# Kernel tuning notes

Measured on AMD Instinct MI355X. Metric: run time of the kernel, lower is better.

Reference implementation:

```python
import jax, jax.numpy as jnp
import numpy as np


def setup_inputs() -> dict:
    key = jax.random.key(0)
    k1, k2, k3, k4 = jax.random.split(key, 4)
    B, S, K, N = 2, 1024, 4096, 4096
    x = jax.random.normal(k1, (B, S, K), dtype=jnp.float32)
    # int8 weights in [-128, 127]
    weight = jax.random.randint(k2, (N, K), -128, 128, dtype=jnp.int8)
    # per-output-channel dequant scales (small positive values)
    scales = jax.random.uniform(k3, (N,), dtype=jnp.float32, minval=0.005, maxval=0.02)
    bias = jax.random.normal(k4, (N,), dtype=jnp.float32) * 0.1
    return {"x": x, "weight": weight, "scales": scales, "bias": bias}


def reference(x, weight, scales, bias):
    # F.linear(x, weight.to(x.dtype)): [B,S,K] @ [N,K]^T -> [B,S,N]
    w = weight.astype(x.dtype)
    y = jnp.einsum('bsk,nk->bsn', x, w)
    # per-output-channel scale + bias epilogue
    return y * scales + bias
```

## Files before the change

kernel.cpp:

```cpp
#include <hip/hip_runtime.h>
#include <hip/hip_bf16.h>
#include <stdint.h>

#define M_DIM 2048
#define N_DIM 4096
#define K_DIM 4096

#define BM 128
#define BN 128
#define BK 128

#define ATILE (BM * BK)
#define BTILE (BN * BK)

typedef __attribute__((ext_vector_type(4))) int   int4v;
typedef __attribute__((ext_vector_type(4))) float f32x4;

__device__ __forceinline__ void load_lds16(const void* g, void* l) {
    __builtin_amdgcn_global_load_lds(
        (const __attribute__((address_space(1))) void*)g,
        (__attribute__((address_space(3))) void*)l,
        16, 0, 0);
}

__global__ __launch_bounds__(256) void quant_x(const float* __restrict__ x,
                                               int8_t* __restrict__ Aq,
                                               float* __restrict__ sx) {
    const int row = blockIdx.x;
    const int tid = threadIdx.x;
    const float4* xr = (const float4*)(x + (size_t)row * K_DIM);

    float4 v[4];
    float mx = 0.f;
#pragma unroll
    for (int p = 0; p < 4; p++) {
        v[p] = xr[p * 256 + tid];
        mx = fmaxf(mx, fmaxf(fmaxf(fabsf(v[p].x), fabsf(v[p].y)),
                             fmaxf(fabsf(v[p].z), fabsf(v[p].w))));
    }
#pragma unroll
    for (int off = 32; off >= 1; off >>= 1)
        mx = fmaxf(mx, __shfl_xor(mx, off, 64));

    __shared__ float wmax[4];
    __shared__ float smax;
    if ((tid & 63) == 0) wmax[tid >> 6] = mx;
    __syncthreads();
    if (tid == 0) {
        float m = fmaxf(fmaxf(wmax[0], wmax[1]), fmaxf(wmax[2], wmax[3]));
        m = fmaxf(m, 1e-20f);
        smax = m;
        sx[row] = m * (1.0f / 127.0f);
    }
    __syncthreads();
    const float inv = 127.0f / smax;

    int* out = (int*)Aq + (size_t)row * (K_DIM / 4);
#pragma unroll
    for (int p = 0; p < 4; p++) {
        int q0 = (int)__builtin_rintf(v[p].x * inv);
        int q1 = (int)__builtin_rintf(v[p].y * inv);
        int q2 = (int)__builtin_rintf(v[p].z * inv);
        int q3 = (int)__builtin_rintf(v[p].w * inv);
        q0 = max(-127, min(127, q0)); q1 = max(-127, min(127, q1));
        q2 = max(-127, min(127, q2)); q3 = max(-127, min(127, q3));
        out[p * 256 + tid] = (q0 & 255) | ((q1 & 255) << 8) |
                             ((q2 & 255) << 16) | ((q3 & 255) << 24);
    }
}

__global__ __launch_bounds__(256) void cvt_w8(const int* __restrict__ w,
                                              int8_t* __restrict__ Bq) {
    size_t i = ((size_t)blockIdx.x * 256 + threadIdx.x) * 16;
    int4 a0 = *(const int4*)(w + i);
    int4 a1 = *(const int4*)(w + i + 4);
    int4 a2 = *(const int4*)(w + i + 8);
    int4 a3 = *(const int4*)(w + i + 12);
    uint4 t;
    t.x = (a0.x & 255) | ((a0.y & 255) << 8) | ((a0.z & 255) << 16) | ((a0.w & 255) << 24);
    t.y = (a1.x & 255) | ((a1.y & 255) << 8) | ((a1.z & 255) << 16) | ((a1.w & 255) << 24);
    t.z = (a2.x & 255) | ((a2.y & 255) << 8) | ((a2.z & 255) << 16) | ((a2.w & 255) << 24);
    t.w = (a3.x & 255) | ((a3.y & 255) << 8) | ((a3.z & 255) << 16) | ((a3.w & 255) << 24);
    *(uint4*)(Bq + i) = t;
}


__global__ __launch_bounds__(512, 4) void gemm_bt_i8(
    const int8_t* __restrict__ A,
    const int8_t* __restrict__ B,
    const float*  __restrict__ sx,
    const float*  __restrict__ scales,
    const float*  __restrict__ bias,
    float* __restrict__ C)
{
    __shared__ __align__(16) int8_t As[2 * ATILE];
    __shared__ __align__(16) int8_t Bs[2 * BTILE];

    const int tid  = threadIdx.x;
    const int bm   = blockIdx.y;
    const int bn   = blockIdx.x;
    const int lane = tid & 63;
    const int wave = tid >> 6;
    const int wm   = (wave >> 2) * 64;
    const int wn   = (wave & 3) * 32;
    const int l16  = lane & 15;
    const int quad = lane >> 4;
    const int swz  = l16 & 7;

    const int srow = tid >> 3;
    const int cgp  = tid & 7;
    const int cgl  = cgp ^ (srow & 7);

    const int8_t* ga0 = A + (size_t)(bm * BM + srow)      * K_DIM + cgl * 16;
    const int8_t* ga1 = A + (size_t)(bm * BM + 64 + srow) * K_DIM + cgl * 16;
    const int8_t* gb0 = B + (size_t)(bn * BN + srow)      * K_DIM + cgl * 16;
    const int8_t* gb1 = B + (size_t)(bn * BN + 64 + srow) * K_DIM + cgl * 16;
    const int la0 = srow * BK + cgp * 16;
    const int la1 = (64 + srow) * BK + cgp * 16;

    load_lds16(ga0, As + la0);
    load_lds16(ga1, As + la1);
    load_lds16(gb0, Bs + la0);
    load_lds16(gb1, Bs + la1);

    int4v acc[4][2] = {};

    int cur = 0;
    for (int k0 = 0; k0 < K_DIM; k0 += BK, cur ^= 1) {
        __syncthreads();

        const int kn = k0 + BK;
        if (kn < K_DIM) {
            const int nb = (cur ^ 1);
            load_lds16(ga0 + kn, As + nb * ATILE + la0);
            load_lds16(ga1 + kn, As + nb * ATILE + la1);
            load_lds16(gb0 + kn, Bs + nb * BTILE + la0);
            load_lds16(gb1 + kn, Bs + nb * BTILE + la1);
        }

        const int8_t* Ab = As + cur * ATILE;
        const int8_t* Bb = Bs + cur * BTILE;

#pragma unroll
        for (int h = 0; h < 2; h++) {
            const int cp = (h * 4 + quad) ^ swz;
            int4v af[4], bfr[2];
#pragma unroll
            for (int i = 0; i < 4; i++)
                af[i] = *(const int4v*)(Ab + (wm + i * 16 + l16) * BK + cp * 16);
#pragma unroll
            for (int j = 0; j < 2; j++)
                bfr[j] = *(const int4v*)(Bb + (wn + j * 16 + l16) * BK + cp * 16);
#pragma unroll
            for (int i = 0; i < 4; i++)
#pragma unroll
                for (int j = 0; j < 2; j++)
                    acc[i][j] = __builtin_amdgcn_mfma_i32_16x16x64_i8(
                        af[i], bfr[j], acc[i][j], 0, 0, 0);
        }
    }

    float sxr[16];
#pragma unroll
    for (int i = 0; i < 4; i++)
#pragma unroll
        for (int r = 0; r < 4; r++)
            sxr[i * 4 + r] = sx[bm * BM + wm + i * 16 + quad * 4 + r];

#pragma unroll
    for (int j = 0; j < 2; j++) {
        const int col = bn * BN + wn + j * 16 + l16;
        const float s = scales[col];
        const float b = bias[col];
#pragma unroll
        for (int i = 0; i < 4; i++) {
            const int row0 = bm * BM + wm + i * 16 + quad * 4;
#pragma unroll
            for (int r = 0; r < 4; r++) {
                C[(size_t)(row0 + r) * N_DIM + col] =
                    (float)acc[i][j][r] * (sxr[i * 4 + r] * s) + b;
            }
        }
    }
}


extern "C" void kernel_launch(void* const* d_in, const int* in_sizes, int n_in,
                              void* d_out, int out_size, void* d_ws, size_t ws_size,
                              hipStream_t stream) {
    const float* x      = (const float*)d_in[0];
    const int*   w      = (const int*)d_in[1];
    const float* scales = (const float*)d_in[2];
    const float* bias   = (const float*)d_in[3];
    float*       out    = (float*)d_out;

    int8_t* Aq = (int8_t*)d_ws;
    int8_t* Bq = (int8_t*)d_ws + (size_t)M_DIM * K_DIM;
    float*  sx = (float*)((int8_t*)d_ws + (size_t)(M_DIM + N_DIM) * K_DIM);

    quant_x<<<M_DIM, 256, 0, stream>>>(x, Aq, sx);
    cvt_w8<<<(int)((size_t)N_DIM * K_DIM / 16 / 256), 256, 0, stream>>>(w, Bq);

    dim3 grid(N_DIM / BN, M_DIM / BM);
    gemm_bt_i8<<<grid, 512, 0, stream>>>(Aq, Bq, sx, scales, bias, out);
}
```

Before: 165.5 us.

## Load A fragments directly to registers and remap blocks per XCD

A fragments are now loaded straight from global memory into registers, double-buffered across two register sets, instead of being staged through LDS. Only B goes through LDS, which halves LDS use and LDS traffic per block. Blocks are launched on a 1D grid and remapped so each XCD gets a contiguous 8x8 group of tiles, aiming for better L2 reuse. The risks are higher register pressure and uncoalesced per-lane global loads for A, since each wave rereads rows that other waves also load.

```diff
diff --git a/kernel.cpp b/kernel.cpp
--- a/kernel.cpp
+++ b/kernel.cpp
@@ -10,8 +10,8 @@
 #define BN 128
 #define BK 128
 
-#define ATILE (BM * BK)
 #define BTILE (BN * BK)
+#define NT (K_DIM / BK)
 
 typedef __attribute__((ext_vector_type(4))) int   int4v;
 typedef __attribute__((ext_vector_type(4))) float f32x4;
@@ -93,12 +93,16 @@
     const float*  __restrict__ bias,
     float* __restrict__ C)
 {
-    __shared__ __align__(16) int8_t As[2 * ATILE];
     __shared__ __align__(16) int8_t Bs[2 * BTILE];
 
     const int tid  = threadIdx.x;
-    const int bm   = blockIdx.y;
-    const int bn   = blockIdx.x;
+
+    const int bid   = blockIdx.x;
+    const int xcd   = bid & 7;
+    const int local = bid >> 3;
+    const int bm    = (xcd >> 2) * 8 + (local >> 3);
+    const int bn    = (xcd & 3) * 8 + (local & 7);
+
     const int lane = tid & 63;
     const int wave = tid >> 6;
     const int wm   = (wave >> 2) * 64;
@@ -108,57 +112,67 @@
     const int swz  = l16 & 7;
 
     const int srow = tid >> 3;
-    const int cgp  = tid & 7;
-    const int cgl  = cgp ^ (srow & 7);
-
-    const int8_t* ga0 = A + (size_t)(bm * BM + srow)      * K_DIM + cgl * 16;
-    const int8_t* ga1 = A + (size_t)(bm * BM + 64 + srow) * K_DIM + cgl * 16;
+    const int cgl  = (tid & 7) ^ (srow & 7);
+
     const int8_t* gb0 = B + (size_t)(bn * BN + srow)      * K_DIM + cgl * 16;
     const int8_t* gb1 = B + (size_t)(bn * BN + 64 + srow) * K_DIM + cgl * 16;
-    const int la0 = srow * BK + cgp * 16;
-    const int la1 = (64 + srow) * BK + cgp * 16;
-
-    load_lds16(ga0, As + la0);
-    load_lds16(ga1, As + la1);
-    load_lds16(gb0, Bs + la0);
-    load_lds16(gb1, Bs + la1);
-
+    const int la = tid * 16;
+
+    const int8_t* Ap = A + (size_t)(bm * BM + wm + l16) * K_DIM + quad * 16;
+
+    int4v afA[2][4], afB[2][4];
     int4v acc[4][2] = {};
 
-    int cur = 0;
-    for (int k0 = 0; k0 < K_DIM; k0 += BK, cur ^= 1) {
+#define PREA(dst, k0_) do {                                                  \
+        _Pragma("unroll")                                                    \
+        for (int h = 0; h < 2; h++)                                          \
+            _Pragma("unroll")                                                \
+            for (int i = 0; i < 4; i++)                                      \
+                dst[h][i] = *(const int4v*)(Ap + (k0_) + i * (16 * K_DIM) + h * 64); \
+    } while (0)
+
+#define STAGEB(slot, k0_) do {                                               \
+        load_lds16(gb0 + (k0_), Bs + (slot) * BTILE + la);                   \
+        load_lds16(gb1 + (k0_), Bs + (slot) * BTILE + 8192 + la);            \
+    } while (0)
+
+#define COMP(af, slot) do {                                                  \
+        const int8_t* Bb = Bs + (slot) * BTILE;                              \
+        _Pragma("unroll")                                                    \
+        for (int h = 0; h < 2; h++) {                                        \
+            const int cp = (h * 4 + quad) ^ swz;                             \
+            int4v bf0 = *(const int4v*)(Bb + (wn + l16) * BK + cp * 16);     \
+            int4v bf1 = *(const int4v*)(Bb + (wn + 16 + l16) * BK + cp * 16);\
+            _Pragma("unroll")                                                \
+            for (int i = 0; i < 4; i++) {                                    \
+                acc[i][0] = __builtin_amdgcn_mfma_i32_16x16x64_i8(           \
+                    af[h][i], bf0, acc[i][0], 0, 0, 0);                      \
+                acc[i][1] = __builtin_amdgcn_mfma_i32_16x16x64_i8(           \
+                    af[h][i], bf1, acc[i][1], 0, 0, 0);                      \
+            }                                                                \
+        }                                                                    \
+    } while (0)
+
+    PREA(afA, 0);
+    STAGEB(0, 0);
+
+    for (int t = 0; t < NT; t += 2) {
         __syncthreads();
-
-        const int kn = k0 + BK;
-        if (kn < K_DIM) {
-            const int nb = (cur ^ 1);
-            load_lds16(ga0 + kn, As + nb * ATILE + la0);
-            load_lds16(ga1 + kn, As + nb * ATILE + la1);
-            load_lds16(gb0 + kn, Bs + nb * BTILE + la0);
-            load_lds16(gb1 + kn, Bs + nb * BTILE + la1);
+        PREA(afB, (t + 1) * BK);
+        STAGEB(1, (t + 1) * BK);
+        COMP(afA, 0);
+
+        __syncthreads();
+        if (t + 2 < NT) {
+            PREA(afA, (t + 2) * BK);
+            STAGEB(0, (t + 2) * BK);
         }
-
-        const int8_t* Ab = As + cur * ATILE;
-        const int8_t* Bb = Bs + cur * BTILE;
-
-#pragma unroll
-        for (int h = 0; h < 2; h++) {
-            const int cp = (h * 4 + quad) ^ swz;
-            int4v af[4], bfr[2];
-#pragma unroll
-            for (int i = 0; i < 4; i++)
-                af[i] = *(const int4v*)(Ab + (wm + i * 16 + l16) * BK + cp * 16);
-#pragma unroll
-            for (int j = 0; j < 2; j++)
-                bfr[j] = *(const int4v*)(Bb + (wn + j * 16 + l16) * BK + cp * 16);
-#pragma unroll
-            for (int i = 0; i < 4; i++)
-#pragma unroll
-                for (int j = 0; j < 2; j++)
-                    acc[i][j] = __builtin_amdgcn_mfma_i32_16x16x64_i8(
-                        af[i], bfr[j], acc[i][j], 0, 0, 0);
-        }
-    }
+        COMP(afB, 1);
+    }
+
+#undef PREA
+#undef STAGEB
+#undef COMP
 
     float sxr[16];
 #pragma unroll
@@ -201,6 +215,5 @@
     quant_x<<<M_DIM, 256, 0, stream>>>(x, Aq, sx);
     cvt_w8<<<(int)((size_t)N_DIM * K_DIM / 16 / 256), 256, 0, stream>>>(w, Bq);
 
-    dim3 grid(N_DIM / BN, M_DIM / BM);
-    gemm_bt_i8<<<grid, 512, 0, stream>>>(Aq, Bq, sx, scales, bias, out);
-}
+    gemm_bt_i8<<<512, 512, 0, stream>>>(Aq, Bq, sx, scales, bias, out);
+}
```

New measurement: 259.5 us. +56.8%, slower.

## Split K across wave pairs with 64x64 warp tiles and XCD-aware block mapping

Applied to the files above, without the earlier changes.

The GEMM now uses four spatial waves, each owning a 64x64 output tile, and two K-halves. Each wave pair splits every 128-wide K tile, and the two halves' accumulators are reduced through LDS at the end. Larger per-wave tiles raise fragment reuse, so fewer LDS reads are needed per MFMA. The grid is flattened to 1D and remapped so blocks on the same XCD share A and B rows for L2 locality. The cost is doubled accumulator registers, an extra LDS reduction with syncs, and an epilogue where only half the waves do the stores.

```diff
diff --git a/kernel.cpp b/kernel.cpp
--- a/kernel.cpp
+++ b/kernel.cpp
@@ -12,6 +12,7 @@
 
 #define ATILE (BM * BK)
 #define BTILE (BN * BK)
+#define NT (K_DIM / BK)
 
 typedef __attribute__((ext_vector_type(4))) int   int4v;
 typedef __attribute__((ext_vector_type(4))) float f32x4;
@@ -97,33 +98,40 @@
     __shared__ __align__(16) int8_t Bs[2 * BTILE];
 
     const int tid  = threadIdx.x;
-    const int bm   = blockIdx.y;
-    const int bn   = blockIdx.x;
+
+    const int bid   = blockIdx.x;
+    const int xcd   = bid & 7;
+    const int local = bid >> 3;
+    const int bm    = (xcd >> 2) * 8 + (local >> 3);
+    const int bn    = (xcd & 3) * 8 + (local & 7);
+
     const int lane = tid & 63;
     const int wave = tid >> 6;
-    const int wm   = (wave >> 2) * 64;
-    const int wn   = (wave & 3) * 32;
+    const int spat = wave & 3;
+    const int ks   = wave >> 2;
+    const int wm   = (spat >> 1) * 64;
+    const int wn   = (spat & 1) * 64;
     const int l16  = lane & 15;
     const int quad = lane >> 4;
     const int swz  = l16 & 7;
+    const int cp   = (ks * 4 + quad) ^ swz;
 
     const int srow = tid >> 3;
-    const int cgp  = tid & 7;
-    const int cgl  = cgp ^ (srow & 7);
+    const int cgl  = (tid & 7) ^ (srow & 7);
 
     const int8_t* ga0 = A + (size_t)(bm * BM + srow)      * K_DIM + cgl * 16;
     const int8_t* ga1 = A + (size_t)(bm * BM + 64 + srow) * K_DIM + cgl * 16;
     const int8_t* gb0 = B + (size_t)(bn * BN + srow)      * K_DIM + cgl * 16;
     const int8_t* gb1 = B + (size_t)(bn * BN + 64 + srow) * K_DIM + cgl * 16;
-    const int la0 = srow * BK + cgp * 16;
-    const int la1 = (64 + srow) * BK + cgp * 16;
+    const int la0 = tid * 16;
+    const int la1 = 8192 + tid * 16;
 
     load_lds16(ga0, As + la0);
     load_lds16(ga1, As + la1);
     load_lds16(gb0, Bs + la0);
     load_lds16(gb1, Bs + la1);
 
-    int4v acc[4][2] = {};
+    int4v acc[4][4] = {};
 
     int cur = 0;
     for (int k0 = 0; k0 < K_DIM; k0 += BK, cur ^= 1) {
@@ -141,44 +149,60 @@
         const int8_t* Ab = As + cur * ATILE;
         const int8_t* Bb = Bs + cur * BTILE;
 
-#pragma unroll
-        for (int h = 0; h < 2; h++) {
-            const int cp = (h * 4 + quad) ^ swz;
-            int4v af[4], bfr[2];
+        int4v af[4];
+#pragma unroll
+        for (int i = 0; i < 4; i++)
+            af[i] = *(const int4v*)(Ab + (wm + i * 16 + l16) * BK + cp * 16);
+#pragma unroll
+        for (int j = 0; j < 4; j++) {
+            int4v bf = *(const int4v*)(Bb + (wn + j * 16 + l16) * BK + cp * 16);
 #pragma unroll
             for (int i = 0; i < 4; i++)
-                af[i] = *(const int4v*)(Ab + (wm + i * 16 + l16) * BK + cp * 16);
-#pragma unroll
-            for (int j = 0; j < 2; j++)
-                bfr[j] = *(const int4v*)(Bb + (wn + j * 16 + l16) * BK + cp * 16);
-#pragma unroll
-            for (int i = 0; i < 4; i++)
-#pragma unroll
-                for (int j = 0; j < 2; j++)
-                    acc[i][j] = __builtin_amdgcn_mfma_i32_16x16x64_i8(
-                        af[i], bfr[j], acc[i][j], 0, 0, 0);
+                acc[i][j] = __builtin_amdgcn_mfma_i32_16x16x64_i8(
+                    af[i], bf, acc[i][j], 0, 0, 0);
         }
     }
 
-    float sxr[16];
-#pragma unroll
-    for (int i = 0; i < 4; i++)
-#pragma unroll
-        for (int r = 0; r < 4; r++)
-            sxr[i * 4 + r] = sx[bm * BM + wm + i * 16 + quad * 4 + r];
-
-#pragma unroll
-    for (int j = 0; j < 2; j++) {
-        const int col = bn * BN + wn + j * 16 + l16;
-        const float s = scales[col];
-        const float b = bias[col];
-#pragma unroll
-        for (int i = 0; i < 4; i++) {
-            const int row0 = bm * BM + wm + i * 16 + quad * 4;
-#pragma unroll
-            for (int r = 0; r < 4; r++) {
-                C[(size_t)(row0 + r) * N_DIM + col] =
-                    (float)acc[i][j][r] * (sxr[i * 4 + r] * s) + b;
+    __syncthreads();
+
+    int8_t* rbase = (spat < 2 ? As : Bs) + (spat & 1) * 16384;
+
+    if (ks == 1) {
+#pragma unroll
+        for (int i = 0; i < 4; i++)
+#pragma unroll
+            for (int j = 0; j < 4; j++)
+                *(int4v*)(rbase + ((i * 4 + j) * 64 + lane) * 16) = acc[i][j];
+    }
+    __syncthreads();
+
+    if (ks == 0) {
+#pragma unroll
+        for (int i = 0; i < 4; i++)
+#pragma unroll
+            for (int j = 0; j < 4; j++)
+                acc[i][j] += *(const int4v*)(rbase + ((i * 4 + j) * 64 + lane) * 16);
+
+        float sxr[16];
+#pragma unroll
+        for (int i = 0; i < 4; i++)
+#pragma unroll
+            for (int r = 0; r < 4; r++)
+                sxr[i * 4 + r] = sx[bm * BM + wm + i * 16 + quad * 4 + r];
+
+#pragma unroll
+        for (int j = 0; j < 4; j++) {
+            const int col = bn * BN + wn + j * 16 + l16;
+            const float s = scales[col];
+            const float b = bias[col];
+#pragma unroll
+            for (int i = 0; i < 4; i++) {
+                const int row0 = bm * BM + wm + i * 16 + quad * 4;
+#pragma unroll
+                for (int r = 0; r < 4; r++) {
+                    C[(size_t)(row0 + r) * N_DIM + col] =
+                        (float)acc[i][j][r] * (sxr[i * 4 + r] * s) + b;
+                }
             }
         }
     }
@@ -201,6 +225,5 @@
     quant_x<<<M_DIM, 256, 0, stream>>>(x, Aq, sx);
     cvt_w8<<<(int)((size_t)N_DIM * K_DIM / 16 / 256), 256, 0, stream>>>(w, Bq);
 
-    dim3 grid(N_DIM / BN, M_DIM / BM);
-    gemm_bt_i8<<<grid, 512, 0, stream>>>(Aq, Bq, sx, scales, bias, out);
-}
+    gemm_bt_i8<<<512, 512, 0, stream>>>(Aq, Bq, sx, scales, bias, out);
+}
```

Measured after the change: 165.0 us. Within noise of the previous version (-0.3%).

## Switch int8 GEMM to 32x32x32 MFMA with wider per-wave fragments

Applied to the files above, without the earlier changes.

Replaces the 16x16x64 int8 MFMA tiling (4x2 tiles per wave) with 32x32x32 int8 MFMA (two 32x32 accumulators per wave). LDS fragment loads are restructured to match, and the epilogue is remapped to the 32x32 output layout. The aim is fewer LDS fragment loads per MFMA and better operand reuse per instruction. The epilogue now reads sx per element instead of preloading it into registers, and the per-wave tile changes shape from 64x32 to a 32-column layout with two row blocks.

```diff
diff --git a/kernel.cpp b/kernel.cpp
--- a/kernel.cpp
+++ b/kernel.cpp
@@ -12,9 +12,11 @@
 
 #define ATILE (BM * BK)
 #define BTILE (BN * BK)
+#define NT (K_DIM / BK)
 
-typedef __attribute__((ext_vector_type(4))) int   int4v;
-typedef __attribute__((ext_vector_type(4))) float f32x4;
+typedef __attribute__((ext_vector_type(4)))  int   int4v;
+typedef __attribute__((ext_vector_type(16))) int   int16v;
+typedef __attribute__((ext_vector_type(4)))  float f32x4;
 
 __device__ __forceinline__ void load_lds16(const void* g, void* l) {
     __builtin_amdgcn_global_load_lds(
@@ -103,27 +105,26 @@
     const int wave = tid >> 6;
     const int wm   = (wave >> 2) * 64;
     const int wn   = (wave & 3) * 32;
-    const int l16  = lane & 15;
-    const int quad = lane >> 4;
-    const int swz  = l16 & 7;
+    const int l32  = lane & 31;
+    const int hi   = lane >> 5;
+    const int swz  = l32 & 7;
 
     const int srow = tid >> 3;
-    const int cgp  = tid & 7;
-    const int cgl  = cgp ^ (srow & 7);
+    const int cgl  = (tid & 7) ^ (srow & 7);
 
     const int8_t* ga0 = A + (size_t)(bm * BM + srow)      * K_DIM + cgl * 16;
     const int8_t* ga1 = A + (size_t)(bm * BM + 64 + srow) * K_DIM + cgl * 16;
     const int8_t* gb0 = B + (size_t)(bn * BN + srow)      * K_DIM + cgl * 16;
     const int8_t* gb1 = B + (size_t)(bn * BN + 64 + srow) * K_DIM + cgl * 16;
-    const int la0 = srow * BK + cgp * 16;
-    const int la1 = (64 + srow) * BK + cgp * 16;
+    const int la0 = tid * 16;
+    const int la1 = 8192 + tid * 16;
 
     load_lds16(ga0, As + la0);
     load_lds16(ga1, As + la1);
     load_lds16(gb0, Bs + la0);
     load_lds16(gb1, Bs + la1);
 
-    int4v acc[4][2] = {};
+    int16v acc[2] = {};
 
     int cur = 0;
     for (int k0 = 0; k0 < K_DIM; k0 += BK, cur ^= 1) {
@@ -141,45 +142,33 @@
         const int8_t* Ab = As + cur * ATILE;
         const int8_t* Bb = Bs + cur * BTILE;
 
+        int4v af[2][4], bf[4];
 #pragma unroll
-        for (int h = 0; h < 2; h++) {
-            const int cp = (h * 4 + quad) ^ swz;
-            int4v af[4], bfr[2];
+        for (int ks = 0; ks < 4; ks++) {
+            const int cp = ((ks * 2 + hi) ^ swz) * 16;
+            af[0][ks] = *(const int4v*)(Ab + (wm + l32) * BK + cp);
+            af[1][ks] = *(const int4v*)(Ab + (wm + 32 + l32) * BK + cp);
+            bf[ks]    = *(const int4v*)(Bb + (wn + l32) * BK + cp);
+        }
 #pragma unroll
-            for (int i = 0; i < 4; i++)
-                af[i] = *(const int4v*)(Ab + (wm + i * 16 + l16) * BK + cp * 16);
-#pragma unroll
-            for (int j = 0; j < 2; j++)
-                bfr[j] = *(const int4v*)(Bb + (wn + j * 16 + l16) * BK + cp * 16);
-#pragma unroll
-            for (int i = 0; i < 4; i++)
-#pragma unroll
-                for (int j = 0; j < 2; j++)
-                    acc[i][j] = __builtin_amdgcn_mfma_i32_16x16x64_i8(
-                        af[i], bfr[j], acc[i][j], 0, 0, 0);
+        for (int ks = 0; ks < 4; ks++) {
+            acc[0] = __builtin_amdgcn_mfma_i32_32x32x32_i8(af[0][ks], bf[ks], acc[0], 0, 0, 0);
+            acc[1] = __builtin_amdgcn_mfma_i32_32x32x32_i8(af[1][ks], bf[ks], acc[1], 0, 0, 0);
         }
     }
 
-    float sxr[16];
-#pragma unroll
-    for (int i = 0; i < 4; i++)
-#pragma unroll
-        for (int r = 0; r < 4; r++)
-            sxr[i * 4 + r] = sx[bm * BM + wm + i * 16 + quad * 4 + r];
+    const int col = bn * BN + wn + l32;
+    const float s = scales[col];
+    const float b = bias[col];
 
 #pragma unroll
-    for (int j = 0; j < 2; j++) {
-        const int col = bn * BN + wn + j * 16 + l16;
-        const float s = scales[col];
-        const float b = bias[col];
+    for (int t = 0; t < 2; t++) {
+        const int rbase = bm * BM + wm + t * 32 + 4 * hi;
 #pragma unroll
-        for (int i = 0; i < 4; i++) {
-            const int row0 = bm * BM + wm + i * 16 + quad * 4;
-#pragma unroll
-            for (int r = 0; r < 4; r++) {
-                C[(size_t)(row0 + r) * N_DIM + col] =
-                    (float)acc[i][j][r] * (sxr[i * 4 + r] * s) + b;
-            }
+        for (int reg = 0; reg < 16; reg++) {
+            const int row = rbase + (reg & 3) + 8 * (reg >> 2);
+            C[(size_t)row * N_DIM + col] =
+                (float)acc[t][reg] * (sx[row] * s) + b;
         }
     }
 }
```

After: 170.9 us. +3.3%, slower.
